# Kernel optimization log

Hardware: AMD Instinct MI355X
Metric: run time of the kernel (lower is better)

## Reference

```python
import jax, jax.numpy as jnp
import numpy as np

N = 50000      # nodes
E = 800000     # edges (avg degree 16)
F_IN = 128
# (d_in, d_out) for the 9 GCNConv layers with width=256, n_layers=3
DIMS = [(128, 128), (128, 192), (192, 256), (256, 256), (256, 256), (256, 256), (256, 192), (192, 128), (128, 1)]
# ReLU after every conv except loop conv i==n_layers-2 (conv idx 4) and the final conv
RELU = [True, True, True, True, False, True, True, True, False]


def setup_inputs() -> dict:
    key = jax.random.key(0)
    ks = jax.random.split(key, 2 + 2 * len(DIMS))
    inp = {
        "x": jax.random.normal(ks[0], (N, F_IN), dtype=jnp.float32),
        "edge_index": jax.random.randint(ks[1], (2, E), 0, N, dtype=jnp.int64),
    }
    for i, (din, dout) in enumerate(DIMS):
        # Glorot-ish init for weights, small random bias (GCNConv has bias=True)
        inp[f"W{i}"] = jax.random.normal(ks[2 + 2 * i], (din, dout), dtype=jnp.float32) / np.float32(np.sqrt(din))
        inp[f"b{i}"] = jax.random.normal(ks[3 + 2 * i], (dout,), dtype=jnp.float32) * 0.01
    return inp


def _gcn_stack(x, src_f, dst_f, norm, Ws, bs):
    h = x
    for i in range(len(Ws)):
        h = h @ Ws[i]                                  # [N, dout] dense transform first (dout <= din mostly)
        msg = h[src_f] * norm[:, None]                 # gather + edge-normalize  [E+N, dout]
        h = jax.ops.segment_sum(msg, dst_f, num_segments=N) + bs[i]
        if RELU[i]:
            h = jax.nn.relu(h)
        # Dropout layers are identity in eval/inference mode.
    return h


def reference(x, edge_index,
              W0, b0, W1, b1, W2, b2, W3, b3, W4, b4, W5, b5, W6, b6, W7, b7, W8, b8):
    src, dst = edge_index[0], edge_index[1]
    loop = jnp.arange(N, dtype=src.dtype)
    # GCNConv default: add self loops, symmetric normalization D^{-1/2}(A+I)D^{-1/2}
    src_f = jnp.concatenate([src, loop])
    dst_f = jnp.concatenate([dst, loop])
    deg = jax.ops.segment_sum(jnp.ones(E + N, dtype=x.dtype), dst_f, num_segments=N)
    dinv = jax.lax.rsqrt(jnp.maximum(deg, 1.0))        # deg >= 1 thanks to self loops
    norm = dinv[src_f] * dinv[dst_f]                   # per-edge coefficient [E+N]
    Ws = [W0, W1, W2, W3, W4, W5, W6, W7, W8]
    bs = [b0, b1, b2, b3, b4, b5, b6, b7, b8]
    return _gcn_stack(x, src_f, dst_f, norm, Ws, bs)   # [N, 1]
```

## Files before the change

kernel.cpp:

```cpp
#include <hip/hip_runtime.h>


#define TPB 256

using bf16x8 = __attribute__((ext_vector_type(8))) __bf16;
using f32x4  = __attribute__((ext_vector_type(4))) float;
using f32x2  = __attribute__((ext_vector_type(2))) float;

__device__ __forceinline__ unsigned bf16rne(float x) {
    unsigned u = __float_as_uint(x);
    return (u + 0x7fffu + ((u >> 16) & 1u)) >> 16;
}

__device__ __forceinline__ void stage16(const unsigned short* g, unsigned short* l) {
#if __has_builtin(__builtin_amdgcn_global_load_lds)
    __builtin_amdgcn_global_load_lds((const __attribute__((address_space(1))) void*)g,
                                     (__attribute__((address_space(3))) void*)l, 16, 0, 0);
#else
    *(uint4*)((char*)l + (threadIdx.x & 63) * 16) = *(const uint4*)g;
#endif
}


__global__ void zinit_kernel(int* cnt, int* fill, int n) {
    int i = blockIdx.x * blockDim.x + threadIdx.x;
    if (i < n) { cnt[i] = 0; fill[i] = 0; }
}

__global__ void count_kernel(const int* __restrict__ dst, int* __restrict__ cnt, int E) {
    int e = blockIdx.x * blockDim.x + threadIdx.x;
    if (e < E) atomicAdd(&cnt[dst[e]], 1);
}


__global__ void blockhist_kernel(const int* __restrict__ cnt, int* __restrict__ localRank,
                                 int* __restrict__ hb, float* __restrict__ dinv,
                                 int n, int nb) {
    __shared__ int h[64];
    int t = threadIdx.x;
    if (t < 64) h[t] = 0;
    __syncthreads();
    int i = blockIdx.x * TPB + t;
    if (i < n) {
        int c = cnt[i];
        dinv[i] = rsqrtf((float)(c + 1));
        int d = c; if (d > 63) d = 63;
        localRank[i] = atomicAdd(&h[d], 1);
    }
    __syncthreads();
    if (t < 64) hb[t * nb + blockIdx.x] = h[t];
}

__global__ __launch_bounds__(256) void sortscan_kernel(int* __restrict__ hb, int nb) {
    __shared__ int sh[64 * 256];
    __shared__ int tot[64], base[64];
    int t = threadIdx.x;
    int total = 64 * nb;
    for (int i = t; i < total; i += 256) sh[i] = hb[i];
    __syncthreads();
    if (t < 64) {
        int run = 0;
        for (int b = 0; b < nb; b++) {
            int v = sh[t * nb + b];
            sh[t * nb + b] = run;
            run += v;
        }
        tot[t] = run;
    }
    __syncthreads();
    if (t == 0) {
        int acc = 0;
        for (int b = 0; b < 64; b++) { base[b] = acc; acc += tot[b]; }
    }
    __syncthreads();
    for (int i = t; i < total; i += 256) hb[i] = sh[i] + base[i / nb];
}

__global__ void scatter2_kernel(const int* __restrict__ cnt,
                                const int* __restrict__ localRank, const int* __restrict__ hb,
                                int* __restrict__ perm, int* __restrict__ pcnt,
                                int* __restrict__ iperm, int n, int nb) {
    int i = blockIdx.x * TPB + threadIdx.x;
    if (i >= n) return;
    int c = cnt[i];
    int d = c; if (d > 63) d = 63;
    int pos = hb[d * nb + blockIdx.x] + localRank[i];
    perm[pos] = i;
    pcnt[pos] = c;
    iperm[i] = pos;
}

__global__ void scan1_kernel(const int* __restrict__ pcnt, int* __restrict__ prowp2,
                             int* __restrict__ bsums, int n) {
    __shared__ int sh[TPB];
    int t = threadIdx.x;
    int i = blockIdx.x * TPB + t;
    int v = (i < n) ? (pcnt[i] + 1) : 0;
    sh[t] = v;
    __syncthreads();
    for (int off = 1; off < TPB; off <<= 1) {
        int x = (t >= off) ? sh[t - off] : 0;
        __syncthreads();
        sh[t] += x;
        __syncthreads();
    }
    if (i < n) prowp2[i] = sh[t] - v;
    if (t == TPB - 1) bsums[blockIdx.x] = sh[t];
}

__global__ void scan2_kernel(int* __restrict__ bsums, int nb) {
    __shared__ int sh[TPB];
    int t = threadIdx.x;
    int v = (t < nb) ? bsums[t] : 0;
    sh[t] = v;
    __syncthreads();
    for (int off = 1; off < TPB; off <<= 1) {
        int x = (t >= off) ? sh[t - off] : 0;
        __syncthreads();
        sh[t] += x;
        __syncthreads();
    }
    if (t < nb) bsums[t] = sh[t] - v;
}

__global__ void scan3_kernel(int* __restrict__ rowp, const int* __restrict__ bsums, int n) {
    int i = blockIdx.x * TPB + threadIdx.x;
    if (i < n) rowp[i] += bsums[blockIdx.x];
}

__global__ void fillself_kernel(const int* __restrict__ src, const int* __restrict__ dst,
                                const float* __restrict__ dinv,
                                const int* __restrict__ iperm, const int* __restrict__ prowp2,
                                int* __restrict__ fill, const int* __restrict__ cnt,
                                unsigned* __restrict__ edges2, int E, int n) {
    int id = blockIdx.x * blockDim.x + threadIdx.x;
    if (id < E) {
        int s = src[id], d = dst[id];
        int pos = prowp2[iperm[d]] + atomicAdd(&fill[d], 1);
        edges2[pos] = (unsigned)s | (bf16rne(dinv[s] * dinv[d]) << 16);
    } else if (id < E + n) {
        int i = id - E;
        float dv = dinv[i];
        edges2[prowp2[iperm[i]] + cnt[i]] = (unsigned)i | (bf16rne(dv * dv) << 16);
    }
}


struct WPtrs { const float* p[8]; };

__global__ void wt_all_kernel(WPtrs wp, unsigned short* __restrict__ Wts) {
    const int cum[9] = {0, 16384, 40960, 90112, 155648, 221184, 286720, 335872, 360448};
    const int Ns[8] = {128, 192, 256, 256, 256, 256, 192, 128};
    const int Ks[8] = {128, 128, 192, 256, 256, 256, 256, 192};
    int id = blockIdx.x * blockDim.x + threadIdx.x;
    if (id >= 360448) return;
    int L = 0;
#pragma unroll
    for (int t = 1; t < 8; t++) if (id >= cum[t]) L = t;
    int lid = id - cum[L];
    int N = Ns[L], K = Ks[L];
    int k = lid / N, n = lid - k * N;
    Wts[cum[L] + n * K + k] = (unsigned short)bf16rne(wp.p[L][lid]);
}

__global__ void cvt_bf16_kernel(const float* __restrict__ in, unsigned short* __restrict__ out,
                                int n4) {
    int i = blockIdx.x * blockDim.x + threadIdx.x;
    if (i >= n4) return;
    float4 v = ((const float4*)in)[i];
    uint2 o;
    o.x = bf16rne(v.x) | (bf16rne(v.y) << 16);
    o.y = bf16rne(v.z) | (bf16rne(v.w) << 16);
    ((uint2*)out)[i] = o;
}


__global__ __launch_bounds__(256) void gemm_mfma_kernel(
    const unsigned short* __restrict__ A, const unsigned short* __restrict__ Wt,
    const float* __restrict__ bias, unsigned short* __restrict__ C,
    int M, int K, int Nc, int doBias, int doRelu, int outChunked) {
    __shared__ unsigned short Qb[128 * 64];
    __shared__ unsigned short Pb[128 * 64];
    int tid = threadIdx.x;
    int l = tid & 63, w = tid >> 6;
    int node0 = blockIdx.x * 128, feat0 = blockIdx.y * 128;

    f32x4 acc[4][4];
#pragma unroll
    for (int i = 0; i < 4; i++)
#pragma unroll
        for (int j = 0; j < 4; j++) acc[i][j] = (f32x4){0.f, 0.f, 0.f, 0.f};

    const unsigned short* gQ[4];
    const unsigned short* gP[4];
    unsigned short* lQ[4];
    unsigned short* lP[4];
#pragma unroll
    for (int h = 0; h < 4; h++) {
        int slot = tid + h * 256;
        int r = slot >> 3, q = slot & 7;
        int qg = q ^ (r & 7);
        int nd = node0 + r; if (nd > M - 1) nd = M - 1;
        int ft = feat0 + r; if (ft > Nc - 1) ft = Nc - 1;
        gQ[h] = A + (size_t)nd * K + qg * 8;
        gP[h] = Wt + (size_t)ft * K + qg * 8;
        lQ[h] = Qb + (size_t)(w * 64 + h * 256) * 8;
        lP[h] = Pb + (size_t)(w * 64 + h * 256) * 8;
    }

    int q4 = l >> 4, m16 = l & 15;
    int featHalf = w & 1, nodeHalf = w >> 1;
    int rP0 = featHalf * 64 + m16;
    int rQ0 = nodeHalf * 64 + m16;
    int sw = m16 & 7;

    for (int k0 = 0; k0 < K; k0 += 64) {
        __syncthreads();
#pragma unroll
        for (int h = 0; h < 4; h++) {
            stage16(gQ[h] + k0, lQ[h]);
            stage16(gP[h] + k0, lP[h]);
        }
        __syncthreads();
#pragma unroll
        for (int ko = 0; ko < 2; ko++) {
            bf16x8 pf[4], qf[4];
#pragma unroll
            for (int i = 0; i < 4; i++)
                pf[i] = *(const bf16x8*)(Pb + (rP0 + i * 16) * 64 + ((ko * 4 + q4) ^ sw) * 8);
#pragma unroll
            for (int j = 0; j < 4; j++)
                qf[j] = *(const bf16x8*)(Qb + (rQ0 + j * 16) * 64 + ((ko * 4 + q4) ^ sw) * 8);
#pragma unroll
            for (int i = 0; i < 4; i++)
#pragma unroll
                for (int j = 0; j < 4; j++)
                    acc[i][j] = __builtin_amdgcn_mfma_f32_16x16x32_bf16(pf[i], qf[j],
                                                                        acc[i][j], 0, 0, 0);
        }
    }

#pragma unroll
    for (int i = 0; i < 4; i++) {
        int gf0 = feat0 + featHalf * 64 + i * 16 + q4 * 4;
        if (gf0 >= Nc) continue;
        float4 bv = make_float4(0.f, 0.f, 0.f, 0.f);
        if (doBias) bv = *(const float4*)(bias + gf0);
        size_t cb = outChunked ? ((size_t)(gf0 >> 5) * ((size_t)M * 32) + (gf0 & 31))
                               : (size_t)gf0;
#pragma unroll
        for (int j = 0; j < 4; j++) {
            int gn = node0 + nodeHalf * 64 + j * 16 + m16;
            if (gn >= M) continue;
            f32x4 v = acc[i][j];
            float x0 = v[0] + bv.x, x1 = v[1] + bv.y;
            float x2 = v[2] + bv.z, x3 = v[3] + bv.w;
            if (doRelu) {
                x0 = fmaxf(x0, 0.f); x1 = fmaxf(x1, 0.f);
                x2 = fmaxf(x2, 0.f); x3 = fmaxf(x3, 0.f);
            }
            uint2 o;
            o.x = bf16rne(x0) | (bf16rne(x1) << 16);
            o.y = bf16rne(x2) | (bf16rne(x3) << 16);
            size_t off = outChunked ? (cb + (size_t)gn * 32) : (cb + (size_t)gn * Nc);
            *(uint2*)(C + off) = o;
        }
    }
}

__global__ void gemv128_bf16_kernel(const unsigned short* __restrict__ A,
                                    const float* __restrict__ w,
                                    float* __restrict__ out, int M) {
    int wid = (blockIdx.x * blockDim.x + threadIdx.x) >> 6;
    int lane = threadIdx.x & 63;
    if (wid >= M) return;
    const unsigned short* a = A + (size_t)wid * 128;
    float a0 = __uint_as_float((unsigned)a[lane] << 16);
    float a1 = __uint_as_float((unsigned)a[lane + 64] << 16);
    float s = a0 * w[lane] + a1 * w[lane + 64];
#pragma unroll
    for (int off = 32; off > 0; off >>= 1) s += __shfl_down(s, off);
    if (lane == 0) out[wid] = s;
}


__global__ __launch_bounds__(256) void agg_group_kernel(
    const uint2* __restrict__ in, const int* __restrict__ prowp2,
    const int* __restrict__ pcnt, const int* __restrict__ perm,
    const unsigned* __restrict__ edges2,
    const float* __restrict__ bias, uint2* __restrict__ out,
    int Q, int upx, int ngPerUnit, int NG, int n_nodes, int rowVec2,
    int doBias, int doRelu, int outChunked) {
    int xcd = blockIdx.x & 7;
    int slot = blockIdx.x >> 3;
    int u = slot / ngPerUnit;
    int ngIdx = slot - u * ngPerUnit;
    int unit = xcd * upx + u;
    int chunk = unit / Q;
    int q = unit - chunk * Q;
    int ng = ngIdx * Q + q;
    if (ng >= NG) return;

    int wave = threadIdx.x >> 6;
    int lane = threadIdx.x & 63;
    int group = lane >> 3, fl = lane & 7;
    int gb = lane & ~7;
    int i = ng * 32 + wave * 8 + group;
    if (i >= n_nodes) return;

    const uint2* slice = in + (size_t)chunk * n_nodes * 8;
    int s0 = prowp2[i];
    int c = pcnt[i] + 1;
    int node = perm[i];

    f32x2 aA[4], aB[4];
#pragma unroll
    for (int k = 0; k < 4; k++) { aA[k] = (f32x2){0.f, 0.f}; aB[k] = (f32x2){0.f, 0.f}; }

    unsigned ew = (fl < c) ? edges2[s0 + fl] : 0u;
    for (int base = 0; base < c; base += 8) {
        int nidx = base + 8 + fl;
        unsigned ewn = (nidx < c) ? edges2[s0 + nidx] : 0u;
        unsigned e[8];
#pragma unroll
        for (int j = 0; j < 8; j++) e[j] = (unsigned)__shfl((int)ew, gb + j);
        uint2 p[8];
#pragma unroll
        for (int j = 0; j < 8; j++) p[j] = slice[(int)(e[j] & 0xffffu) * 8 + fl];
#pragma unroll
        for (int j = 0; j < 8; j++) {
            float wgt = __uint_as_float(e[j] & 0xffff0000u);
            int k = j & 3;
            f32x2 v0 = {__uint_as_float(p[j].x << 16),
                        __uint_as_float(p[j].x & 0xffff0000u)};
            f32x2 v1 = {__uint_as_float(p[j].y << 16),
                        __uint_as_float(p[j].y & 0xffff0000u)};
            f32x2 w2 = {wgt, wgt};
            aA[k] += w2 * v0;
            aB[k] += w2 * v1;
        }
        ew = ewn;
    }
    f32x2 sA = (aA[0] + aA[1]) + (aA[2] + aA[3]);
    f32x2 sB = (aB[0] + aB[1]) + (aB[2] + aB[3]);

    if (doBias) {
        float4 bb = ((const float4*)bias)[chunk * 8 + fl];
        sA += (f32x2){bb.x, bb.y};
        sB += (f32x2){bb.z, bb.w};
    }
    if (doRelu) {
        sA[0] = fmaxf(sA[0], 0.f); sA[1] = fmaxf(sA[1], 0.f);
        sB[0] = fmaxf(sB[0], 0.f); sB[1] = fmaxf(sB[1], 0.f);
    }
    uint2 o;
    o.x = bf16rne(sA[0]) | (bf16rne(sA[1]) << 16);
    o.y = bf16rne(sB[0]) | (bf16rne(sB[1]) << 16);
    size_t oi = outChunked ? ((size_t)chunk * n_nodes * 8 + (size_t)node * 8 + fl)
                           : ((size_t)node * rowVec2 + chunk * 8 + fl);
    out[oi] = o;
}

__global__ void agg1_kernel(const float* __restrict__ in, const int* __restrict__ prowp2,
                            const int* __restrict__ pcnt, const int* __restrict__ perm,
                            const unsigned* __restrict__ edges2,
                            const float* __restrict__ bias, float* __restrict__ out,
                            int n_nodes) {
    int n = blockIdx.x * blockDim.x + threadIdx.x;
    if (n >= n_nodes) return;
    float acc = 0.f;
    int s0 = prowp2[n];
    int c = pcnt[n] + 1;
    for (int j = 0; j < c; j++) {
        unsigned e = edges2[s0 + j];
        acc += __uint_as_float(e & 0xffff0000u) * in[e & 0xffffu];
    }
    acc += bias[0];
    out[perm[n]] = acc;
}


extern "C" void kernel_launch(void* const* d_in, const int* in_sizes, int n_in,
                              void* d_out, int out_size, void* d_ws, size_t ws_size,
                              hipStream_t stream) {
    const float* x = (const float*)d_in[0];
    const int* ei = (const int*)d_in[1];
    const int Nn = in_sizes[0] / 128;
    const int E = in_sizes[1] / 2;
    const int* src = ei;
    const int* dst = ei + E;

    char* ws = (char*)d_ws;
    size_t off = 0;
    auto alloc = [&](size_t bytes) -> char* {
        char* p = ws + off;
        off = (off + bytes + 255) & ~(size_t)255;
        return p;
    };
    int* cnt = (int*)alloc((size_t)Nn * 4);
    int* fill = (int*)alloc((size_t)Nn * 4);
    int* bsums = (int*)alloc(1024);
    float* dinv = (float*)alloc((size_t)Nn * 4);
    int* localRank = (int*)alloc((size_t)Nn * 4);
    int* hb = (int*)alloc((size_t)64 * 256 * 4);
    int* perm = (int*)alloc((size_t)Nn * 4);
    int* pcnt = (int*)alloc((size_t)Nn * 4);
    int* iperm = (int*)alloc((size_t)Nn * 4);
    int* prowp2 = (int*)alloc((size_t)Nn * 4);
    unsigned* edges2 = (unsigned*)alloc((size_t)(E + Nn + 64) * 4);
    unsigned short* T = (unsigned short*)alloc((size_t)Nn * 256 * 2);
    unsigned short* H = (unsigned short*)alloc((size_t)Nn * 256 * 2);
    unsigned short* Bx = (unsigned short*)alloc((size_t)Nn * 128 * 2);
    float* F = (float*)alloc((size_t)Nn * 4);
    unsigned short* Wts = (unsigned short*)alloc((size_t)400000 * 2);
    (void)ws_size;

    const int dims[9][2] = {{128,128},{128,192},{192,256},{256,256},{256,256},
                            {256,256},{256,192},{192,128},{128,1}};
    unsigned short* Wt[8];
    {
        size_t o = 0;
        for (int i = 0; i < 8; i++) { Wt[i] = Wts + o; o += (size_t)dims[i][0] * dims[i][1]; }
    }

    int nbN = (Nn + TPB - 1) / TPB;
    int nbE = (E + TPB - 1) / TPB;
    int nbEN = (E + Nn + TPB - 1) / TPB;

    zinit_kernel<<<nbN, TPB, 0, stream>>>(cnt, fill, Nn);
    count_kernel<<<nbE, TPB, 0, stream>>>(dst, cnt, E);
    blockhist_kernel<<<nbN, TPB, 0, stream>>>(cnt, localRank, hb, dinv, Nn, nbN);
    sortscan_kernel<<<1, 256, 0, stream>>>(hb, nbN);
    scatter2_kernel<<<nbN, TPB, 0, stream>>>(cnt, localRank, hb, perm, pcnt, iperm,
                                             Nn, nbN);
    scan1_kernel<<<nbN, TPB, 0, stream>>>(pcnt, prowp2, bsums, Nn);
    scan2_kernel<<<1, TPB, 0, stream>>>(bsums, nbN);
    scan3_kernel<<<nbN, TPB, 0, stream>>>(prowp2, bsums, Nn);
    fillself_kernel<<<nbEN, TPB, 0, stream>>>(src, dst, dinv, iperm, prowp2, fill, cnt,
                                              edges2, E, Nn);

    WPtrs wp;
    for (int i = 0; i < 8; i++) wp.p[i] = (const float*)d_in[2 + 2 * i];
    wt_all_kernel<<<(360448 + TPB - 1) / TPB, TPB, 0, stream>>>(wp, Wts);
    cvt_bf16_kernel<<<(Nn * 32 + TPB - 1) / TPB, TPB, 0, stream>>>(x, Bx, Nn * 32);

    auto gemm = [&](const unsigned short* A, int i, unsigned short* C, int K, int Nc,
                    int doBias, int doRelu, int outChunked) {
        const float* b = (const float*)d_in[3 + 2 * i];
        dim3 grid((Nn + 127) / 128, (Nc + 127) / 128);
        gemm_mfma_kernel<<<grid, 256, 0, stream>>>(A, Wt[i], b, C, Nn, K, Nc,
                                                   doBias, doRelu, outChunked);
    };
    int NG = (Nn + 31) / 32;
    auto agg = [&](const unsigned short* inb, unsigned short* outb, int w, int i,
                   int doBias, int doRelu, int outChunked) {
        int nch = w / 32;
        int Q = (nch == 8) ? 1 : (nch == 6) ? 4 : 2;
        int upx = nch * Q / 8;
        int ngPerUnit = (NG + Q - 1) / Q;
        int blocksPerXcd = upx * ngPerUnit;
        const float* b = (const float*)d_in[3 + 2 * i];
        agg_group_kernel<<<blocksPerXcd * 8, 256, 0, stream>>>(
            (const uint2*)inb, prowp2, pcnt, perm, edges2, b, (uint2*)outb,
            Q, upx, ngPerUnit, NG, Nn, w / 4, doBias, doRelu, outChunked);
    };

    gemm(Bx, 0, T, 128, 128, 0, 0, 1);
    agg(T, H, 128, 0, 1, 1, 1);
    agg(H, T, 128, 1, 0, 0, 0);
    gemm(T, 1, H, 128, 192, 1, 1, 1);
    agg(H, T, 192, 2, 0, 0, 0);
    gemm(T, 2, H, 192, 256, 1, 1, 0);
    gemm(H, 3, T, 256, 256, 0, 0, 1);
    agg(T, H, 256, 3, 1, 1, 0);
    gemm(H, 4, T, 256, 256, 0, 0, 1);
    agg(T, H, 256, 4, 1, 0, 0);
    gemm(H, 5, T, 256, 256, 0, 0, 1);
    agg(T, H, 256, 5, 1, 1, 0);
    gemm(H, 6, T, 256, 192, 0, 0, 1);
    agg(T, H, 192, 6, 1, 1, 0);
    gemm(H, 7, T, 192, 128, 0, 0, 1);
    agg(T, H, 128, 7, 1, 1, 0);
    gemv128_bf16_kernel<<<(Nn + 3) / 4, 256, 0, stream>>>(H, (const float*)d_in[2 + 16],
                                                          F, Nn);
    agg1_kernel<<<nbN, TPB, 0, stream>>>(F, prowp2, pcnt, perm, edges2,
                                         (const float*)d_in[3 + 16], (float*)d_out, Nn);
}
```

Measured before the change: 655.7 us.

## Aggregate all feature chunks per node in one block with 64-wide chunked layout

Replaces the per-chunk aggregation kernel, which scheduled 32-feature chunks across XCDs, with a templated kernel where each 8-lane group handles every 64-feature chunk of a node in one pass. The GEMM's chunked output layout widens from 32 to 64 features per chunk, so each lane loads 16 bytes per chunk. This reads edge lists and indices once per node instead of once per chunk and issues wider loads. In exchange it uses more registers per thread and drops the XCD-aware L2 partitioning of the feature slices, and blocks are launched in reverse node-group order.

```diff
diff --git a/kernel.cpp b/kernel.cpp
--- a/kernel.cpp
+++ b/kernel.cpp
@@ -10,6 +10,10 @@
 __device__ __forceinline__ unsigned bf16rne(float x) {
     unsigned u = __float_as_uint(x);
     return (u + 0x7fffu + ((u >> 16) & 1u)) >> 16;
+}
+
+__device__ __forceinline__ f32x2 bl2(unsigned u) {
+    return (f32x2){__uint_as_float(u << 16), __uint_as_float(u & 0xffff0000u)};
 }
 
 __device__ __forceinline__ void stage16(const unsigned short* g, unsigned short* l) {
@@ -246,7 +250,7 @@
         if (gf0 >= Nc) continue;
         float4 bv = make_float4(0.f, 0.f, 0.f, 0.f);
         if (doBias) bv = *(const float4*)(bias + gf0);
-        size_t cb = outChunked ? ((size_t)(gf0 >> 5) * ((size_t)M * 32) + (gf0 & 31))
+        size_t cb = outChunked ? ((size_t)(gf0 >> 6) * ((size_t)M * 64) + (gf0 & 63))
                                : (size_t)gf0;
 #pragma unroll
         for (int j = 0; j < 4; j++) {
@@ -262,7 +266,7 @@
             uint2 o;
             o.x = bf16rne(x0) | (bf16rne(x1) << 16);
             o.y = bf16rne(x2) | (bf16rne(x3) << 16);
-            size_t off = outChunked ? (cb + (size_t)gn * 32) : (cb + (size_t)gn * Nc);
+            size_t off = outChunked ? (cb + (size_t)gn * 64) : (cb + (size_t)gn * Nc);
             *(uint2*)(C + off) = o;
         }
     }
@@ -284,38 +288,30 @@
 }
 
 
-__global__ __launch_bounds__(256) void agg_group_kernel(
-    const uint2* __restrict__ in, const int* __restrict__ prowp2,
+template<int NC>
+__global__ __launch_bounds__(256) void agg_all_kernel(
+    const uint4* __restrict__ in, const int* __restrict__ prowp2,
     const int* __restrict__ pcnt, const int* __restrict__ perm,
-    const unsigned* __restrict__ edges2,
-    const float* __restrict__ bias, uint2* __restrict__ out,
-    int Q, int upx, int ngPerUnit, int NG, int n_nodes, int rowVec2,
+    const unsigned* __restrict__ edges2, const float* __restrict__ bias,
+    uint4* __restrict__ out, int NG, int n_nodes,
     int doBias, int doRelu, int outChunked) {
-    int xcd = blockIdx.x & 7;
-    int slot = blockIdx.x >> 3;
-    int u = slot / ngPerUnit;
-    int ngIdx = slot - u * ngPerUnit;
-    int unit = xcd * upx + u;
-    int chunk = unit / Q;
-    int q = unit - chunk * Q;
-    int ng = ngIdx * Q + q;
-    if (ng >= NG) return;
-
+    int bid = NG - 1 - (int)blockIdx.x;
     int wave = threadIdx.x >> 6;
     int lane = threadIdx.x & 63;
     int group = lane >> 3, fl = lane & 7;
     int gb = lane & ~7;
-    int i = ng * 32 + wave * 8 + group;
+    int i = bid * 32 + wave * 8 + group;
     if (i >= n_nodes) return;
 
-    const uint2* slice = in + (size_t)chunk * n_nodes * 8;
     int s0 = prowp2[i];
     int c = pcnt[i] + 1;
     int node = perm[i];
 
-    f32x2 aA[4], aB[4];
-#pragma unroll
-    for (int k = 0; k < 4; k++) { aA[k] = (f32x2){0.f, 0.f}; aB[k] = (f32x2){0.f, 0.f}; }
+    f32x2 a[NC][4];
+#pragma unroll
+    for (int ch = 0; ch < NC; ch++)
+#pragma unroll
+        for (int k = 0; k < 4; k++) a[ch][k] = (f32x2){0.f, 0.f};
 
     unsigned ew = (fl < c) ? edges2[s0 + fl] : 0u;
     for (int base = 0; base < c; base += 8) {
@@ -324,41 +320,56 @@
         unsigned e[8];
 #pragma unroll
         for (int j = 0; j < 8; j++) e[j] = (unsigned)__shfl((int)ew, gb + j);
-        uint2 p[8];
-#pragma unroll
-        for (int j = 0; j < 8; j++) p[j] = slice[(int)(e[j] & 0xffffu) * 8 + fl];
 #pragma unroll
         for (int j = 0; j < 8; j++) {
+            int so = (int)(e[j] & 0xffffu) * 8 + fl;
             float wgt = __uint_as_float(e[j] & 0xffff0000u);
-            int k = j & 3;
-            f32x2 v0 = {__uint_as_float(p[j].x << 16),
-                        __uint_as_float(p[j].x & 0xffff0000u)};
-            f32x2 v1 = {__uint_as_float(p[j].y << 16),
-                        __uint_as_float(p[j].y & 0xffff0000u)};
             f32x2 w2 = {wgt, wgt};
-            aA[k] += w2 * v0;
-            aB[k] += w2 * v1;
+            uint4 p[NC];
+#pragma unroll
+            for (int ch = 0; ch < NC; ch++)
+                p[ch] = in[(size_t)ch * n_nodes * 8 + so];
+#pragma unroll
+            for (int ch = 0; ch < NC; ch++) {
+                a[ch][0] += w2 * bl2(p[ch].x);
+                a[ch][1] += w2 * bl2(p[ch].y);
+                a[ch][2] += w2 * bl2(p[ch].z);
+                a[ch][3] += w2 * bl2(p[ch].w);
+            }
         }
         ew = ewn;
     }
-    f32x2 sA = (aA[0] + aA[1]) + (aA[2] + aA[3]);
-    f32x2 sB = (aB[0] + aB[1]) + (aB[2] + aB[3]);
-
-    if (doBias) {
-        float4 bb = ((const float4*)bias)[chunk * 8 + fl];
-        sA += (f32x2){bb.x, bb.y};
-        sB += (f32x2){bb.z, bb.w};
-    }
-    if (doRelu) {
-        sA[0] = fmaxf(sA[0], 0.f); sA[1] = fmaxf(sA[1], 0.f);
-        sB[0] = fmaxf(sB[0], 0.f); sB[1] = fmaxf(sB[1], 0.f);
-    }
-    uint2 o;
-    o.x = bf16rne(sA[0]) | (bf16rne(sA[1]) << 16);
-    o.y = bf16rne(sB[0]) | (bf16rne(sB[1]) << 16);
-    size_t oi = outChunked ? ((size_t)chunk * n_nodes * 8 + (size_t)node * 8 + fl)
-                           : ((size_t)node * rowVec2 + chunk * 8 + fl);
-    out[oi] = o;
+
+#pragma unroll
+    for (int ch = 0; ch < NC; ch++) {
+        f32x2 s[4];
+#pragma unroll
+        for (int k = 0; k < 4; k++) s[k] = a[ch][k];
+        if (doBias) {
+            const float* bp = bias + ch * 64 + fl * 8;
+            float4 b0 = *(const float4*)bp;
+            float4 b1 = *(const float4*)(bp + 4);
+            s[0] += (f32x2){b0.x, b0.y};
+            s[1] += (f32x2){b0.z, b0.w};
+            s[2] += (f32x2){b1.x, b1.y};
+            s[3] += (f32x2){b1.z, b1.w};
+        }
+        if (doRelu) {
+#pragma unroll
+            for (int k = 0; k < 4; k++) {
+                s[k][0] = fmaxf(s[k][0], 0.f);
+                s[k][1] = fmaxf(s[k][1], 0.f);
+            }
+        }
+        uint4 o;
+        o.x = bf16rne(s[0][0]) | (bf16rne(s[0][1]) << 16);
+        o.y = bf16rne(s[1][0]) | (bf16rne(s[1][1]) << 16);
+        o.z = bf16rne(s[2][0]) | (bf16rne(s[2][1]) << 16);
+        o.w = bf16rne(s[3][0]) | (bf16rne(s[3][1]) << 16);
+        size_t oi = outChunked ? ((size_t)ch * n_nodes * 8 + (size_t)node * 8 + fl)
+                               : ((size_t)node * (NC * 8) + ch * 8 + fl);
+        out[oi] = o;
+    }
 }
 
 __global__ void agg1_kernel(const float* __restrict__ in, const int* __restrict__ prowp2,
@@ -454,15 +465,16 @@
     int NG = (Nn + 31) / 32;
     auto agg = [&](const unsigned short* inb, unsigned short* outb, int w, int i,
                    int doBias, int doRelu, int outChunked) {
-        int nch = w / 32;
-        int Q = (nch == 8) ? 1 : (nch == 6) ? 4 : 2;
-        int upx = nch * Q / 8;
-        int ngPerUnit = (NG + Q - 1) / Q;
-        int blocksPerXcd = upx * ngPerUnit;
         const float* b = (const float*)d_in[3 + 2 * i];
-        agg_group_kernel<<<blocksPerXcd * 8, 256, 0, stream>>>(
-            (const uint2*)inb, prowp2, pcnt, perm, edges2, b, (uint2*)outb,
-            Q, upx, ngPerUnit, NG, Nn, w / 4, doBias, doRelu, outChunked);
+        if (w == 256)
+            agg_all_kernel<4><<<NG, 256, 0, stream>>>((const uint4*)inb, prowp2, pcnt,
+                perm, edges2, b, (uint4*)outb, NG, Nn, doBias, doRelu, outChunked);
+        else if (w == 192)
+            agg_all_kernel<3><<<NG, 256, 0, stream>>>((const uint4*)inb, prowp2, pcnt,
+                perm, edges2, b, (uint4*)outb, NG, Nn, doBias, doRelu, outChunked);
+        else
+            agg_all_kernel<2><<<NG, 256, 0, stream>>>((const uint4*)inb, prowp2, pcnt,
+                perm, edges2, b, (uint4*)outb, NG, Nn, doBias, doRelu, outChunked);
     };
 
     gemm(Bx, 0, T, 128, 128, 0, 0, 1);
```

Measured after the change: 726.8 us. +10.9%, slower.
